# Performance work log

Measured on AMD Instinct MI355X. Metric: run time of the kernel, lower is better.

The kernel has to match this reference:

```python
import jax, jax.numpy as jnp
import numpy as np

N, E = 50000, 800000
IN, MAP, H, O = 256, 64, 4, 64
LEAKY_SLOPE = 0.2


def setup_inputs() -> dict:
    key = jax.random.key(0)
    ks = jax.random.split(key, 12)
    x = jax.random.normal(ks[0], (N, IN), dtype=jnp.float32)
    src = jax.random.randint(ks[1], (E,), 0, N, dtype=jnp.int32)
    dst = jax.random.randint(ks[2], (E,), 0, N, dtype=jnp.int32)
    s = 1.0 / np.sqrt(IN)
    W_gat = jax.random.normal(ks[3], (IN, H * O), dtype=jnp.float32) * s
    attn_l = jax.random.normal(ks[4], (H, O), dtype=jnp.float32) * 0.1
    attn_r = jax.random.normal(ks[5], (H, O), dtype=jnp.float32) * 0.1
    gate_m_W = jax.random.normal(ks[6], (IN, MAP), dtype=jnp.float32) * s
    gate_m_b = jnp.zeros((MAP,), dtype=jnp.float32)
    gate_fn_W = jax.random.normal(ks[7], (2 * IN + MAP, H), dtype=jnp.float32) * (1.0 / np.sqrt(2 * IN + MAP))
    gate_fn_b = jnp.zeros((H,), dtype=jnp.float32)
    merge_W = jax.random.normal(ks[8], (IN + O, O), dtype=jnp.float32) * (1.0 / np.sqrt(IN + O))
    merge_b = jnp.zeros((O,), dtype=jnp.float32)
    return {"x": x, "src": src, "dst": dst, "W_gat": W_gat, "attn_l": attn_l,
            "attn_r": attn_r, "gate_m_W": gate_m_W, "gate_m_b": gate_m_b,
            "gate_fn_W": gate_fn_W, "gate_fn_b": gate_fn_b,
            "merge_W": merge_W, "merge_b": merge_b}


def _forward(x, src, dst, W_gat, attn_l, attn_r, gate_m_W, gate_m_b,
             gate_fn_W, gate_fn_b, merge_W, merge_b):
    n = x.shape[0]
    # --- gate branch: gspmm mean of x, gspmm max of linear_z over in-neighbors ---
    deg = jax.ops.segment_sum(jnp.ones_like(dst, dtype=x.dtype), dst, num_segments=n)
    mean_z = jax.ops.segment_sum(x[src], dst, num_segments=n) / jnp.maximum(deg, 1.0)[:, None]
    z = x @ gate_m_W + gate_m_b  # [N, MAP]
    max_z = jax.ops.segment_max(z[src], dst, num_segments=n)
    max_z = jnp.where(deg[:, None] > 0, max_z, 0.0)  # empty neighborhoods -> 0
    nft = jnp.concatenate([x, max_z, mean_z], axis=1)  # [N, 2*IN+MAP]
    gate = jax.nn.sigmoid(nft @ gate_fn_W + gate_fn_b)  # [N, H]
    # --- GATConv ---
    feat = (x @ W_gat).reshape(n, H, O)  # [N, H, O]
    el = jnp.einsum('nho,ho->nh', feat, attn_l)
    er = jnp.einsum('nho,ho->nh', feat, attn_r)
    e = jax.nn.leaky_relu(el[src] + er[dst], negative_slope=LEAKY_SLOPE)  # [E, H]
    m = jax.ops.segment_max(e, dst, num_segments=n)  # [N, H]
    m = jnp.where(jnp.isfinite(m), m, 0.0)
    ex = jnp.exp(e - m[dst])  # [E, H]
    s = jax.ops.segment_sum(ex, dst, num_segments=n)  # [N, H]
    alpha = ex / jnp.maximum(s[dst], 1e-16)  # [E, H]
    attn_out = jax.ops.segment_sum(feat[src] * alpha[:, :, None], dst, num_segments=n)  # [N, H, O]
    # --- gated merge ---
    gated = (gate[:, :, None] * attn_out).mean(axis=1)  # [N, O]
    merge = jnp.concatenate([x, gated], axis=1) @ merge_W + merge_b  # [N, O]
    return merge


def reference(x, src, dst, W_gat, attn_l, attn_r, gate_m_W, gate_m_b,
              gate_fn_W, gate_fn_b, merge_W, merge_b):
    return _forward(x, src, dst, W_gat, attn_l, attn_r, gate_m_W, gate_m_b,
                    gate_fn_W, gate_fn_b, merge_W, merge_b)
```

## Files before the change

### kernel.cpp

```cpp
#include <hip/hip_runtime.h>
#include <math.h>

#define NN 50000
#define NE 800000
#define LEAKY 0.2f
#define NT 26
#define CAP 96
#define NBT (8 * NT * 64)
#define PREP_BLKS 251
#define FUSE_BLKS 4692

typedef short bf16x8 __attribute__((ext_vector_type(8)));
typedef float f32x4 __attribute__((ext_vector_type(4)));
typedef float f32x2 __attribute__((ext_vector_type(2)));

__device__ __forceinline__ unsigned short f2bf(float f) {
  unsigned u = __float_as_uint(f);
  u += 0x7fffu + ((u >> 16) & 1u);
  return (unsigned short)(u >> 16);
}
__device__ __forceinline__ float leaky(float v) { return v > 0.0f ? v : LEAKY * v; }
__device__ __forceinline__ float rlf(float v, int l) {
  return __uint_as_float(__builtin_amdgcn_readlane(__float_as_uint(v), l));
}
__device__ __forceinline__ int rli(int v, int l) {
  return __builtin_amdgcn_readlane(v, l);
}

__device__ __forceinline__ bf16x8 cvt8(float4 fa, float4 fb) {
  unsigned r0, r1, r2, r3;
  asm("v_cvt_pk_bf16_f32 %0, %1, %2" : "=v"(r0) : "v"(fa.x), "v"(fa.y));
  asm("v_cvt_pk_bf16_f32 %0, %1, %2" : "=v"(r1) : "v"(fa.z), "v"(fa.w));
  asm("v_cvt_pk_bf16_f32 %0, %1, %2" : "=v"(r2) : "v"(fb.x), "v"(fb.y));
  asm("v_cvt_pk_bf16_f32 %0, %1, %2" : "=v"(r3) : "v"(fb.z), "v"(fb.w));
  union { uint4 u; bf16x8 v; } c;
  c.u = make_uint4(r0, r1, r2, r3);
  return c.v;
}

#if defined(__has_builtin)
#if __has_builtin(__builtin_amdgcn_cvt_pk_f32_fp8) && \
    __has_builtin(__builtin_amdgcn_cvt_pk_fp8_f32) && \
    __has_builtin(__builtin_amdgcn_cvt_f32_fp8)
#define FP8_HW 1
#endif
#endif

#ifdef FP8_HW
__device__ __forceinline__ unsigned char f2fp8(float v) {
  return (unsigned char)(__builtin_amdgcn_cvt_pk_fp8_f32(v, v, 0u, false) & 0xFF);
}
__device__ __forceinline__ f32x2 fp8x2_lo(unsigned int v) {
  return __builtin_amdgcn_cvt_pk_f32_fp8(v, false);
}
__device__ __forceinline__ f32x2 fp8x2_hi(unsigned int v) {
  return __builtin_amdgcn_cvt_pk_f32_fp8(v, true);
}
__device__ __forceinline__ float fp8one(unsigned int v) {
  return __builtin_amdgcn_cvt_f32_fp8(v, 0);
}
#else
__device__ __forceinline__ unsigned char f2fp8(float f) {
  unsigned u = __float_as_uint(f);
  unsigned s = (u >> 31) << 7;
  unsigned a = u & 0x7FFFFFFFu;
  if (a >= 0x43E00000u) return (unsigned char)(s | 0x7E);
  if (a < 0x3C800000u) {
    float m = __uint_as_float(a) * 512.0f;
    int q = (int)(m + 0.5f); if (q > 7) q = 7;
    return (unsigned char)(s | q);
  }
  a += 0x7FFFFu + ((a >> 20) & 1);
  unsigned e = ((a >> 23) & 0xFF) - 120;
  if (e > 15) return (unsigned char)(s | 0x7E);
  return (unsigned char)(s | (e << 3) | ((a >> 20) & 7));
}
__device__ __forceinline__ float fp8dec1(unsigned b) {
  unsigned s = (b & 0x80u) << 24;
  unsigned em = b & 0x7Fu;
  unsigned e4 = em >> 3, m3 = em & 7;
  float v = e4 ? __uint_as_float(((e4 + 120) << 23) | (m3 << 20))
               : (float)m3 * 0.001953125f;
  return __uint_as_float(__float_as_uint(v) ^ s);
}
__device__ __forceinline__ f32x2 fp8x2_lo(unsigned int v) {
  f32x2 r; r[0] = fp8dec1(v & 0xFF); r[1] = fp8dec1((v >> 8) & 0xFF); return r;
}
__device__ __forceinline__ f32x2 fp8x2_hi(unsigned int v) {
  f32x2 r; r[0] = fp8dec1((v >> 16) & 0xFF); r[1] = fp8dec1((v >> 24) & 0xFF); return r;
}
__device__ __forceinline__ float fp8one(unsigned int v) { return fp8dec1(v & 0xFF); }
#endif

__device__ __forceinline__ float panel_w(int col, int k,
    const float* W_gat, const float* gate_m_W, const float* merge_W,
    const float* gate_fn_W, const float* attn_l, const float* attn_r) {
  if (col < 256)      return W_gat[k * 256 + (col & 3) * 64 + (col >> 2)];
  else if (col < 320) return gate_m_W[k * 64 + (col - 256)];
  else if (col < 384) return merge_W[k * 64 + (col - 320)];
  else if (col < 388) return gate_fn_W[k * 4 + (col - 384)];
  else if (col < 392) return gate_fn_W[(320 + k) * 4 + (col - 388)];
  else if (col < 396) {
    int h = col - 392; float s = 0.0f;
    for (int o = 0; o < 64; ++o) s += W_gat[k * 256 + h * 64 + o] * attn_l[h * 64 + o];
    return s;
  } else if (col < 400) {
    int h = col - 396; float s = 0.0f;
    for (int o = 0; o < 64; ++o) s += W_gat[k * 256 + h * 64 + o] * attn_r[h * 64 + o];
    return s;
  }
  return 0.0f;
}

__global__ __launch_bounds__(256) void k_prep(
    const float* __restrict__ W_gat, const float* __restrict__ gate_m_W,
    const float* __restrict__ merge_W, const float* __restrict__ gate_fn_W,
    const float* __restrict__ attn_l, const float* __restrict__ attn_r,
    unsigned short* __restrict__ Btf, unsigned short* __restrict__ mWf,
    unsigned char* __restrict__ zq, float* __restrict__ epay,
    unsigned char* __restrict__ featq, int* __restrict__ cursor) {
  int b = blockIdx.x, tid = threadIdx.x;
  if (b < 54) {
    int idx = b * 256 + tid;
    if (idx < NBT) {
      int kq = idx / (NT * 64);
      int rem = idx - kq * (NT * 64);
      int t = rem >> 6, lane = rem & 63;
      int col = t * 16 + (lane & 15);
      int k = kq * 32 + (lane >> 4) * 8;
      unsigned short* o = Btf + (size_t)idx * 8;
#pragma unroll
      for (int i = 0; i < 8; ++i)
        o[i] = f2bf(panel_w(col, k + i, W_gat, gate_m_W, merge_W, gate_fn_W,
                            attn_l, attn_r));
    } else {
      int idx2 = idx - NBT;
      int kq = idx2 >> 8;
      int rem = idx2 & 255;
      int t = rem >> 6, lane = rem & 63;
      int col = t * 16 + (lane & 15);
      int k = kq * 32 + ((lane >> 4) & 3) * 8;
      unsigned short* o = mWf + (size_t)idx2 * 8;
#pragma unroll
      for (int i = 0; i < 8; ++i)
        o[i] = f2bf(merge_W[(size_t)(256 + k + i) * 64 + col]);
    }
  } else if (b == 54) {
    if (tid < 64) zq[(size_t)NN * 64 + tid] = 0xFE;
    if (tid < 8) epay[(size_t)NN * 8 + tid] = 0.0f;
    featq[(size_t)NN * 256 + tid] = 0;
  } else {
    int i = (b - 55) * 256 + tid;
    if (i < NN) cursor[i] = 0;
  }
}

__global__ __launch_bounds__(256, 3) void k_gemm_scatter(
    const float* __restrict__ x, const unsigned short* __restrict__ Btf,
    const float* __restrict__ gate_m_b,
    unsigned char* __restrict__ featq, unsigned char* __restrict__ zq,
    float* __restrict__ xm, float* __restrict__ gx, float* __restrict__ epay,
    float* __restrict__ erv,
    const int* __restrict__ src, const int* __restrict__ dst,
    int* __restrict__ cursor, unsigned short* __restrict__ csr_src) {
  __shared__ unsigned short ldsB[2][13][64][8];
  int bq = blockIdx.x / 3, br = blockIdx.x % 3;
  if (br != 0) {
    int sIdx = bq * 2 + (br - 1);
    int e = sIdx * 256 + threadIdx.x;
    if (e < NE) {
      int n = dst[e];
      int pos = atomicAdd(&cursor[n], 1);
      if (pos < CAP) csr_src[n * CAP + pos] = (unsigned short)src[e];
    }
    return;
  }
  int rb = bq >> 1, ch = bq & 1;
  int lane = threadIdx.x & 63, wave = threadIdx.x >> 6;
  int m = lane & 15, kg = lane >> 4;
  int rowB = rb * 64;
  int t0 = ch * 13;
  int arow = rowB + wave * 16 + m;
  if (arow >= NN) arow = NN - 1;
  const float* aP = x + (size_t)arow * 256 + kg * 8;

  f32x4 acc[13];
  f32x4 zero = {0.f, 0.f, 0.f, 0.f};
#pragma unroll
  for (int t = 0; t < 13; ++t) acc[t] = zero;

  for (int t = wave; t < 13; t += 4)
    __builtin_amdgcn_global_load_lds(
        (const __attribute__((address_space(1))) unsigned int*)
            (Btf + ((size_t)(t0 + t)) * 512 + lane * 8),
        (__attribute__((address_space(3))) unsigned int*)(&ldsB[0][t][0][0]),
        16, 0, 0);
  float4 fa = *(const float4*)aP;
  float4 fb = *(const float4*)(aP + 4);
  __syncthreads();

#pragma unroll 1
  for (int kq = 0; kq < 8; ++kq) {
    int cur = kq & 1;
    int kqn = kq < 7 ? kq + 1 : 7;
    float4 fa_n = *(const float4*)(aP + kqn * 32);
    float4 fb_n = *(const float4*)(aP + kqn * 32 + 4);
    if (kq < 7) {
      for (int t = wave; t < 13; t += 4)
        __builtin_amdgcn_global_load_lds(
            (const __attribute__((address_space(1))) unsigned int*)
                (Btf + ((size_t)(kq + 1) * NT + t0 + t) * 512 + lane * 8),
            (__attribute__((address_space(3))) unsigned int*)
                (&ldsB[cur ^ 1][t][0][0]),
            16, 0, 0);
    }
    bf16x8 a = cvt8(fa, fb);
#pragma unroll
    for (int t = 0; t < 13; ++t) {
      bf16x8 bfr = *(const bf16x8*)&ldsB[cur][t][lane][0];
      acc[t] = __builtin_amdgcn_mfma_f32_16x16x32_bf16(a, bfr, acc[t], 0, 0, 0);
    }
    fa = fa_n; fb = fb_n;
    __syncthreads();
  }

  if (ch == 0) {
#pragma unroll
    for (int r = 0; r < 4; ++r) {
      int row = rowB + wave * 16 + kg * 4 + r;
      if (row >= NN) continue;
#pragma unroll
      for (int t = 0; t < 13; ++t)
        featq[(size_t)row * 256 + t * 16 + m] = f2fp8(acc[t][r]);
    }
  } else {
#pragma unroll
    for (int r = 0; r < 4; ++r) {
      int row = rowB + wave * 16 + kg * 4 + r;
      if (row >= NN) continue;
#pragma unroll
      for (int t = 0; t < 3; ++t)
        featq[(size_t)row * 256 + 208 + t * 16 + m] = f2fp8(acc[t][r]);
#pragma unroll
      for (int t = 3; t < 7; ++t) {
        int cc = (t - 3) * 16 + m;
        zq[(size_t)row * 64 + cc] = f2fp8(acc[t][r] + gate_m_b[cc]);
      }
#pragma unroll
      for (int t = 7; t < 11; ++t)
        xm[(size_t)row * 64 + (t - 7) * 16 + m] = acc[t][r];
      float v = acc[11][r];
      if (m < 4)       gx[(size_t)row * 4 + m] = v;
      else if (m < 8)  epay[(size_t)row * 8 + (m - 4) * 2 + 1] = v;
      else if (m < 12) epay[(size_t)row * 8 + (m - 8) * 2] = v;
      else             erv[(size_t)row * 4 + (m - 12)] = v;
    }
  }
}

__global__ __launch_bounds__(256) void k_node(
    const unsigned char* __restrict__ zq, const unsigned char* __restrict__ featq,
    const float* __restrict__ epay, const float* __restrict__ er,
    const float* __restrict__ gx,
    const int* __restrict__ cursor, const unsigned short* __restrict__ csr_src,
    const float* __restrict__ gate_fn_W, const float* __restrict__ gate_fn_b,
    const unsigned short* __restrict__ mWf, const float* __restrict__ xm,
    const float* __restrict__ merge_b, float* __restrict__ out) {
  __shared__ float WzT[4][64];
  __shared__ float pbuf[4][16][4];
  __shared__ unsigned short gLDS[16][72];
  int tid = threadIdx.x;
  {
    int c = tid >> 2, h = tid & 3;
    WzT[h][c] = gate_fn_W[(256 + c) * 4 + h];
  }
  __syncthreads();

  int lane = tid & 63, wave = tid >> 6;
  int hh = lane >> 4, le = lane & 15;
  int rowbase = blockIdx.x * 16;
  int nodeBase = rowbase + wave * 4;
#pragma unroll 1
  for (int i = 0; i < 4; ++i) {
    int node = nodeBase + i;
    int deg = cursor[node]; if (deg > CAP) deg = CAP;
    float gated = 0.0f;
    if (deg > 0) {
      int rs = node * CAP, re = rs + deg;
      float er_h = er[(size_t)node * 4 + hh];
      f32x2 A01 = {0.f, 0.f}, A23 = {0.f, 0.f};
      float psum = 0, usum = 0;
      float mz = -INFINITY;
      int jj = rs + le;
      int s_l = (jj < re) ? (int)csr_src[jj] : NN;
#pragma unroll 1
      for (int j0 = rs; j0 < re; j0 += 16) {
        int jn = j0 + 16 + le;
        int s_nx = (jn < re) ? (int)csr_src[jn] : NN;
        bool valid = (j0 + le) < re;
        float2 eu = *(const float2*)(epay + ((size_t)(unsigned)s_l << 3) + hh * 2);
        float p = valid ? __expf(leaky(eu.x + er_h)) : 0.0f;
        psum += p;
        usum += eu.y;
        pbuf[wave][le][hh] = p;
        unsigned int fvr[16];
        unsigned int zvr[16];
#pragma unroll
        for (int e2 = 0; e2 < 16; ++e2) {
          int s = rli(s_l, e2);
          fvr[e2] = *(const unsigned int*)(featq + ((size_t)(unsigned)s << 8) + lane * 4);
        }
#pragma unroll
        for (int e2 = 0; e2 < 16; ++e2) {
          int s = rli(s_l, e2);
          zvr[e2] = zq[((size_t)(unsigned)s << 6) + lane];
        }
#pragma unroll
        for (int e2 = 0; e2 < 16; ++e2) {
          float4 pv = *(const float4*)pbuf[wave][e2];
          f32x2 p01 = {pv.x, pv.y};
          f32x2 p23 = {pv.z, pv.w};
          A01 += p01 * fp8x2_lo(fvr[e2]);
          A23 += p23 * fp8x2_hi(fvr[e2]);
          mz = fmaxf(mz, fp8one(zvr[e2]));
        }
        s_l = s_nx;
      }
#pragma unroll
      for (int off = 1; off < 16; off <<= 1) {
        psum += __shfl_xor(psum, off, 64);
        usum += __shfl_xor(usum, off, 64);
      }
      float s0 = rlf(psum, 0),  s1 = rlf(psum, 16);
      float s2 = rlf(psum, 32), s3 = rlf(psum, 48);
      float su0 = rlf(usum, 0),  su1 = rlf(usum, 16);
      float su2 = rlf(usum, 32), su3 = rlf(usum, 48);

      float g[4];
#pragma unroll
      for (int h = 0; h < 4; ++h) {
        float t = mz * WzT[h][lane];
#pragma unroll
        for (int off = 32; off; off >>= 1) t += __shfl_xor(t, off, 64);
        g[h] = t;
      }
      float inv_deg = 1.0f / (float)deg;
      float4 gx4 = *(const float4*)(gx + (size_t)node * 4);
      float g0 = 1.0f / (1.0f + __expf(-(g[0] + gx4.x + su0 * inv_deg + gate_fn_b[0])));
      float g1 = 1.0f / (1.0f + __expf(-(g[1] + gx4.y + su1 * inv_deg + gate_fn_b[1])));
      float g2 = 1.0f / (1.0f + __expf(-(g[2] + gx4.z + su2 * inv_deg + gate_fn_b[2])));
      float g3 = 1.0f / (1.0f + __expf(-(g[3] + gx4.w + su3 * inv_deg + gate_fn_b[3])));
      gated = 0.25f * (g0 * A01[0] / s0 + g1 * A01[1] / s1 +
                       g2 * A23[0] / s2 + g3 * A23[1] / s3);
    }
    gLDS[wave * 4 + i][lane] = f2bf(gated);
  }
  __syncthreads();

  int m = lane & 15, kg = lane >> 4;
  f32x4 acc = {0.f, 0.f, 0.f, 0.f};
#pragma unroll
  for (int kq = 0; kq < 2; ++kq) {
    bf16x8 a = *(const bf16x8*)(&gLDS[m][kq * 32 + kg * 8]);
    bf16x8 b = *(const bf16x8*)(mWf + (((size_t)kq * 4 + wave) * 64 + lane) * 8);
    acc = __builtin_amdgcn_mfma_f32_16x16x32_bf16(a, b, acc, 0, 0, 0);
  }
  int c = wave * 16 + m;
  float mb = merge_b[c];
#pragma unroll
  for (int r = 0; r < 4; ++r) {
    int row = rowbase + kg * 4 + r;
    out[(size_t)row * 64 + c] = acc[r] + xm[(size_t)row * 64 + c] + mb;
  }
}

extern "C" void kernel_launch(void* const* d_in, const int* in_sizes, int n_in,
                              void* d_out, int out_size, void* d_ws, size_t ws_size,
                              hipStream_t stream) {
  const float* x         = (const float*)d_in[0];
  const int*   src       = (const int*)d_in[1];
  const int*   dst       = (const int*)d_in[2];
  const float* W_gat     = (const float*)d_in[3];
  const float* attn_l    = (const float*)d_in[4];
  const float* attn_r    = (const float*)d_in[5];
  const float* gate_m_W  = (const float*)d_in[6];
  const float* gate_m_b  = (const float*)d_in[7];
  const float* gate_fn_W = (const float*)d_in[8];
  const float* gate_fn_b = (const float*)d_in[9];
  const float* merge_W   = (const float*)d_in[10];
  const float* merge_b   = (const float*)d_in[11];
  float* out = (float*)d_out;

  char* ws = (char*)d_ws;
  size_t off = 0;
  auto alloc = [&](size_t bytes) -> void* {
    off = (off + 255) & ~(size_t)255;
    void* p = ws + off;
    off += bytes;
    return p;
  };
  int* cursor    = (int*)alloc((size_t)NN * 4);
  unsigned short* csr_src = (unsigned short*)alloc((size_t)NN * CAP * 2);
  float* epay = (float*)alloc((size_t)(NN + 1) * 8 * 4);
  float* er   = (float*)alloc((size_t)NN * 4 * 4);
  float* gx   = (float*)alloc((size_t)NN * 4 * 4);
  float* xm   = (float*)alloc((size_t)NN * 64 * 4);
  unsigned char* zq    = (unsigned char*)alloc((size_t)(NN + 1) * 64);
  unsigned char* featq = (unsigned char*)alloc((size_t)(NN + 1) * 256);
  unsigned short* Btf    = (unsigned short*)alloc((size_t)NBT * 8 * 2);
  unsigned short* mWf    = (unsigned short*)alloc((size_t)512 * 8 * 2);

  k_prep<<<PREP_BLKS, 256, 0, stream>>>(W_gat, gate_m_W, merge_W, gate_fn_W,
                                        attn_l, attn_r, Btf, mWf, zq, epay,
                                        featq, cursor);
  k_gemm_scatter<<<FUSE_BLKS, 256, 0, stream>>>(x, Btf, gate_m_b,
                                                featq, zq, xm, gx, epay, er,
                                                src, dst, cursor, csr_src);
  k_node<<<NN / 16, 256, 0, stream>>>(zq, featq, epay, er, gx, cursor, csr_src,
                                      gate_fn_W, gate_fn_b, mWf, xm, merge_b, out);
}
```

Before: 253.1 us.

## Partition CSR scatter by destination-node class aligned to XCD block mapping

Scatter blocks now each scan a chunk of edges but only insert edges whose destination falls in one of 8 node classes, chosen as blockIdx & 7. Because blocks are dealt round-robin across the 8 XCDs, this keeps atomics and CSR writes for a node range on a single XCD's L2. The aim is to cut cross-die atomic traffic and cache-line bouncing, at the cost of each edge's dst being read by 8 blocks. It also vectorizes the attention-weight dot products in the prep panel and grows the grid with early exit for unused GEMM blocks.

```diff
diff --git a/kernel.cpp b/kernel.cpp
--- a/kernel.cpp
+++ b/kernel.cpp
@@ -8,7 +8,10 @@
 #define CAP 96
 #define NBT (8 * NT * 64)
 #define PREP_BLKS 251
-#define FUSE_BLKS 4692
+#define FUSE_BLKS 4704
+#define GEMM_USED 1564
+#define SCHUNK 2041
+#define NODES_PER_CLASS 6250
 
 typedef short bf16x8 __attribute__((ext_vector_type(8)));
 typedef float f32x4 __attribute__((ext_vector_type(4)));
@@ -92,6 +95,18 @@
 __device__ __forceinline__ float fp8one(unsigned int v) { return fp8dec1(v & 0xFF); }
 #endif
 
+__device__ __forceinline__ float dot64v(const float* __restrict__ w,
+                                        const float* __restrict__ a) {
+  float4 p0 = {0.f, 0.f, 0.f, 0.f};
+#pragma unroll
+  for (int o = 0; o < 64; o += 4) {
+    float4 wv = *(const float4*)(w + o);
+    float4 av = *(const float4*)(a + o);
+    p0.x += wv.x * av.x; p0.y += wv.y * av.y;
+    p0.z += wv.z * av.z; p0.w += wv.w * av.w;
+  }
+  return (p0.x + p0.y) + (p0.z + p0.w);
+}
 __device__ __forceinline__ float panel_w(int col, int k,
     const float* W_gat, const float* gate_m_W, const float* merge_W,
     const float* gate_fn_W, const float* attn_l, const float* attn_r) {
@@ -101,13 +116,11 @@
   else if (col < 388) return gate_fn_W[k * 4 + (col - 384)];
   else if (col < 392) return gate_fn_W[(320 + k) * 4 + (col - 388)];
   else if (col < 396) {
-    int h = col - 392; float s = 0.0f;
-    for (int o = 0; o < 64; ++o) s += W_gat[k * 256 + h * 64 + o] * attn_l[h * 64 + o];
-    return s;
+    int h = col - 392;
+    return dot64v(W_gat + k * 256 + h * 64, attn_l + h * 64);
   } else if (col < 400) {
-    int h = col - 396; float s = 0.0f;
-    for (int o = 0; o < 64; ++o) s += W_gat[k * 256 + h * 64 + o] * attn_r[h * 64 + o];
-    return s;
+    int h = col - 396;
+    return dot64v(W_gat + k * 256 + h * 64, attn_r + h * 64);
   }
   return 0.0f;
 }
@@ -164,17 +177,30 @@
     const int* __restrict__ src, const int* __restrict__ dst,
     int* __restrict__ cursor, unsigned short* __restrict__ csr_src) {
   __shared__ unsigned short ldsB[2][13][64][8];
-  int bq = blockIdx.x / 3, br = blockIdx.x % 3;
+  int br = blockIdx.x % 3;
   if (br != 0) {
-    int sIdx = bq * 2 + (br - 1);
-    int e = sIdx * 256 + threadIdx.x;
-    if (e < NE) {
+    int c = blockIdx.x & 7;
+    int w24 = blockIdx.x / 24, r = blockIdx.x % 24;
+    int q0 = c, q1 = c + 8, q2 = c + 16;
+    int a1;
+    if (q0 % 3 == 0)      { a1 = q2; }
+    else if (q1 % 3 == 0) { a1 = q2; }
+    else                  { a1 = q1; }
+    int chunk = w24 * 2 + (r == a1 ? 1 : 0);
+    int lo = c * NODES_PER_CLASS, hi = lo + NODES_PER_CLASS;
+    int base = chunk * SCHUNK;
+    int end = base + SCHUNK; if (end > NE) end = NE;
+    for (int e = base + threadIdx.x; e < end; e += 256) {
       int n = dst[e];
-      int pos = atomicAdd(&cursor[n], 1);
-      if (pos < CAP) csr_src[n * CAP + pos] = (unsigned short)src[e];
+      if (n >= lo && n < hi) {
+        int pos = atomicAdd(&cursor[n], 1);
+        if (pos < CAP) csr_src[n * CAP + pos] = (unsigned short)src[e];
+      }
     }
     return;
   }
+  int bq = blockIdx.x / 3;
+  if (bq >= GEMM_USED) return;
   int rb = bq >> 1, ch = bq & 1;
   int lane = threadIdx.x & 63, wave = threadIdx.x >> 6;
   int m = lane & 15, kg = lane >> 4;
```

Result: faster. 245.9 us (-2.9%).
